# Optimization experiments

Hardware: AMD Instinct MI355X
Metric: run time of the kernel (lower is better)

The kernel has to match this reference:

```python
import jax, jax.numpy as jnp
import numpy as np

GROUPS = 32
HEADS = 8
EPS = 1e-5


def setup_inputs() -> dict:
    key = jax.random.key(0)
    ks = jax.random.split(key, 3)
    b, c, h, w = 8, 512, 32, 32
    x = jax.random.normal(ks[0], (b, c, h, w), dtype=jnp.float32)
    gn_w = jnp.ones((c,), jnp.float32)
    gn_b = jnp.zeros((c,), jnp.float32)
    qkv_w = jax.random.normal(ks[1], (3 * c, c), dtype=jnp.float32) * (1.0 / np.sqrt(c))
    qkv_b = jnp.zeros((3 * c,), jnp.float32)
    proj_w = jax.random.normal(ks[2], (c, c), dtype=jnp.float32) * (1.0 / np.sqrt(c))
    proj_b = jnp.zeros((c,), jnp.float32)
    return {"x": x, "gn_w": gn_w, "gn_b": gn_b, "qkv_w": qkv_w,
            "qkv_b": qkv_b, "proj_w": proj_w, "proj_b": proj_b}


def group_norm(x, weight, bias):
    b, c, h, w = x.shape
    xg = x.reshape(b, GROUPS, c // GROUPS, h, w)
    mean = xg.mean(axis=(2, 3, 4), keepdims=True)
    var = xg.var(axis=(2, 3, 4), keepdims=True)
    xn = ((xg - mean) * jax.lax.rsqrt(var + EPS)).reshape(b, c, h, w)
    return xn * weight[None, :, None, None] + bias[None, :, None, None]


def reference(x, gn_w, gn_b, qkv_w, qkv_b, proj_w, proj_b):
    b, c, h, w = x.shape
    dh = c // HEADS
    xn = group_norm(x, gn_w, gn_b)
    # 1x1 conv == per-pixel linear: (b,c,h,w) x (3c,c) -> (b,3c,h,w)
    qkv = jnp.einsum('bchw,oc->bohw', xn, qkv_w) + qkv_b[None, :, None, None]
    qkv = qkv.reshape(b, 3, HEADS, dh, h * w)  # 'three' outermost, then heads, head_dim
    q, k, v = qkv[:, 0], qkv[:, 1], qkv[:, 2]  # (b, heads, dh, hw)
    scale = dh ** (-0.5)
    attn = jax.nn.softmax(jnp.einsum('bhci,bhcj->bhij', q, k) * scale, axis=-1)
    out = jnp.einsum('bhij,bhcj->bhci', attn, v)  # (b, heads, dh, hw)
    out = out.reshape(b, c, h, w)
    out = jnp.einsum('bchw,oc->bohw', out, proj_w) + proj_b[None, :, None, None]
    return x + out
```

## Files before the change

### kernel.cpp

```cpp
#include <hip/hip_runtime.h>
#include <cstdint>
#include <cstddef>

#define BATCH 8
#define CCH   512
#define SSP   1024
#define NH    8
#define DH    64
#define O3    1536

typedef __bf16 bf16x8 __attribute__((ext_vector_type(8)));
typedef float  f32x4  __attribute__((ext_vector_type(4)));

__device__ __forceinline__ unsigned short f2bf(float f) {
    unsigned u = __builtin_bit_cast(unsigned, f);
    unsigned r = u + 0x7fffu + ((u >> 16) & 1u);
    return (unsigned short)(r >> 16);
}

__device__ __forceinline__ unsigned pk2bf(float lo, float hi) {
    unsigned ul = __builtin_bit_cast(unsigned, lo) + 0x8000u;
    unsigned uh = __builtin_bit_cast(unsigned, hi) + 0x8000u;
    return __builtin_amdgcn_perm(uh, ul, 0x07060302u);
}

__device__ __forceinline__ bf16x8 ld8(const unsigned short* p) {
    uint4 u = *(const uint4*)p;
    return __builtin_bit_cast(bf16x8, u);
}

__global__ __launch_bounds__(256) void wconv(const float* __restrict__ src,
                                             unsigned short* __restrict__ dst,
                                             int n4) {
    int i = blockIdx.x * 256 + threadIdx.x;
    if (i < n4) {
        float4 v = ((const float4*)src)[i];
        ushort4 o;
        o.x = f2bf(v.x); o.y = f2bf(v.y); o.z = f2bf(v.z); o.w = f2bf(v.w);
        ((ushort4*)dst)[i] = o;
    }
}

__global__ __launch_bounds__(256) void groupnorm_t(const float* __restrict__ x,
                                                   const float* __restrict__ gw,
                                                   const float* __restrict__ gb,
                                                   unsigned short* __restrict__ xnt) {
    int blk = blockIdx.x;
    int b = blk >> 5, g = blk & 31;
    const float4* xp = (const float4*)(x + (size_t)(b * CCH + g * 16) * SSP);
    int t = threadIdx.x;

    float4 vals[16];
    float sum = 0.f, ss = 0.f;
#pragma unroll
    for (int i = 0; i < 16; i++) {
        float4 v = xp[i * 256 + t];
        vals[i] = v;
        sum += (v.x + v.y) + (v.z + v.w);
        ss  += (v.x * v.x + v.y * v.y) + (v.z * v.z + v.w * v.w);
    }
#pragma unroll
    for (int o = 32; o; o >>= 1) {
        sum += __shfl_xor(sum, o, 64);
        ss  += __shfl_xor(ss,  o, 64);
    }
    __shared__ float red[8];
    if ((t & 63) == 0) { red[(t >> 6) * 2] = sum; red[(t >> 6) * 2 + 1] = ss; }
    __syncthreads();
    sum = red[0] + red[2] + red[4] + red[6];
    ss  = red[1] + red[3] + red[5] + red[7];

    float mean = sum * (1.f / 16384.f);
    float var  = ss * (1.f / 16384.f) - mean * mean;
    float rstd = rsqrtf(var + 1e-5f);

    __shared__ unsigned short tile[16][1032];
#pragma unroll
    for (int i = 0; i < 16; i++) {
        int f4 = i * 256 + t;
        int c = f4 >> 8;
        int s = (f4 & 255) * 4;
        float wsc = gw[g * 16 + c] * rstd;
        float bia = gb[g * 16 + c] - mean * wsc;
        float4 v = vals[i];
        tile[c][s + 0] = f2bf(v.x * wsc + bia);
        tile[c][s + 1] = f2bf(v.y * wsc + bia);
        tile[c][s + 2] = f2bf(v.z * wsc + bia);
        tile[c][s + 3] = f2bf(v.w * wsc + bia);
    }
    __syncthreads();

    int c2 = (t & 7) * 2, sr = t >> 3;
    unsigned short* outbase = xnt + (size_t)b * SSP * CCH + g * 16 + c2;
#pragma unroll
    for (int i = 0; i < 32; i++) {
        int s = i * 32 + sr;
        unsigned v = (unsigned)tile[c2][s] | ((unsigned)tile[c2 + 1][s] << 16);
        *(unsigned*)(outbase + (size_t)s * CCH) = v;
    }
}

__global__ __launch_bounds__(256) void gemm_qkv(const unsigned short* __restrict__ Aall,
                                                const unsigned short* __restrict__ Bw,
                                                const float* __restrict__ bias,
                                                unsigned short* __restrict__ Call) {
    const int K = 512;
    int bz = blockIdx.z;
    const unsigned short* A = Aall + (size_t)bz * SSP * CCH;
    unsigned short* Cp = Call + (size_t)bz * SSP * O3;
    int m0 = blockIdx.x * 128, n0 = blockIdx.y * 128;

    __shared__ unsigned short As[128][40], Bs[128][40];
    int t = threadIdx.x, wave = t >> 6, lane = t & 63;
    int quad = lane >> 4, l16 = lane & 15;
    int wm = (wave & 1) * 64, wn = (wave >> 1) * 64;

    f32x4 acc[4][4];
#pragma unroll
    for (int i = 0; i < 4; i++)
#pragma unroll
        for (int j = 0; j < 4; j++) acc[i][j] = f32x4{0.f, 0.f, 0.f, 0.f};

    int srow = t >> 2, scg = (t & 3) * 8;
    for (int k0 = 0; k0 < K; k0 += 32) {
        __syncthreads();
        *(uint4*)&As[srow][scg]      = *(const uint4*)(A  + (size_t)(m0 + srow) * K + k0 + scg);
        *(uint4*)&As[srow + 64][scg] = *(const uint4*)(A  + (size_t)(m0 + srow + 64) * K + k0 + scg);
        *(uint4*)&Bs[srow][scg]      = *(const uint4*)(Bw + (size_t)(n0 + srow) * K + k0 + scg);
        *(uint4*)&Bs[srow + 64][scg] = *(const uint4*)(Bw + (size_t)(n0 + srow + 64) * K + k0 + scg);
        __syncthreads();
        bf16x8 af[4], bfr[4];
#pragma unroll
        for (int i = 0; i < 4; i++) {
            af[i]  = ld8(&As[wm + i * 16 + l16][quad * 8]);
            bfr[i] = ld8(&Bs[wn + i * 16 + l16][quad * 8]);
        }
#pragma unroll
        for (int i = 0; i < 4; i++)
#pragma unroll
            for (int j = 0; j < 4; j++)
                acc[i][j] = __builtin_amdgcn_mfma_f32_16x16x32_bf16(af[i], bfr[j], acc[i][j], 0, 0, 0);
    }
#pragma unroll
    for (int i = 0; i < 4; i++)
#pragma unroll
        for (int j = 0; j < 4; j++) {
            int col = n0 + wn + j * 16 + l16;
            float bv = bias[col];
#pragma unroll
            for (int r = 0; r < 4; r++) {
                int row = m0 + wm + i * 16 + quad * 4 + r;
                Cp[(size_t)row * O3 + col] = f2bf(acc[i][j][r] + bv);
            }
        }
}

__global__ __launch_bounds__(256) void gemm_proj(const unsigned short* __restrict__ Pw,
                                                 const unsigned short* __restrict__ Oall,
                                                 const float* __restrict__ bias,
                                                 const float* __restrict__ xres,
                                                 float* __restrict__ Out) {
    const int K = 512;
    int bz = blockIdx.z;
    const unsigned short* Bv = Oall + (size_t)bz * SSP * CCH;
    int m0 = blockIdx.x * 128, n0 = blockIdx.y * 128;

    __shared__ unsigned short As[128][40], Bs[128][40];
    int t = threadIdx.x, wave = t >> 6, lane = t & 63;
    int quad = lane >> 4, l16 = lane & 15;
    int wm = (wave & 1) * 64, wn = (wave >> 1) * 64;

    f32x4 acc[4][4];
#pragma unroll
    for (int i = 0; i < 4; i++)
#pragma unroll
        for (int j = 0; j < 4; j++) acc[i][j] = f32x4{0.f, 0.f, 0.f, 0.f};

    int srow = t >> 2, scg = (t & 3) * 8;
    for (int k0 = 0; k0 < K; k0 += 32) {
        __syncthreads();
        *(uint4*)&As[srow][scg]      = *(const uint4*)(Pw + (size_t)(m0 + srow) * K + k0 + scg);
        *(uint4*)&As[srow + 64][scg] = *(const uint4*)(Pw + (size_t)(m0 + srow + 64) * K + k0 + scg);
        *(uint4*)&Bs[srow][scg]      = *(const uint4*)(Bv + (size_t)(n0 + srow) * K + k0 + scg);
        *(uint4*)&Bs[srow + 64][scg] = *(const uint4*)(Bv + (size_t)(n0 + srow + 64) * K + k0 + scg);
        __syncthreads();
        bf16x8 af[4], bfr[4];
#pragma unroll
        for (int i = 0; i < 4; i++) {
            af[i]  = ld8(&As[wm + i * 16 + l16][quad * 8]);
            bfr[i] = ld8(&Bs[wn + i * 16 + l16][quad * 8]);
        }
#pragma unroll
        for (int i = 0; i < 4; i++)
#pragma unroll
            for (int j = 0; j < 4; j++)
                acc[i][j] = __builtin_amdgcn_mfma_f32_16x16x32_bf16(af[i], bfr[j], acc[i][j], 0, 0, 0);
    }
#pragma unroll
    for (int i = 0; i < 4; i++)
#pragma unroll
        for (int j = 0; j < 4; j++) {
            int col = n0 + wn + j * 16 + l16;
#pragma unroll
            for (int r = 0; r < 4; r++) {
                int row = m0 + wm + i * 16 + quad * 4 + r;
                size_t idx = (size_t)bz * CCH * SSP + (size_t)row * SSP + col;
                Out[idx] = xres[idx] + acc[i][j][r] + bias[row];
            }
        }
}

__global__ __launch_bounds__(256) void vtrans(const unsigned short* __restrict__ qkvt,
                                              unsigned short* __restrict__ vt) {
    int j0 = blockIdx.x * 64;
    int bh = blockIdx.y;
    int b = bh >> 3, h = bh & 7;
    __shared__ unsigned short tl[64][72];
    int t = threadIdx.x;
#pragma unroll
    for (int p = 0; p < 2; p++) {
        int jr = p * 32 + (t >> 3), c8 = (t & 7) * 8;
        *(uint4*)&tl[jr][c8] =
            *(const uint4*)(qkvt + ((size_t)b * SSP + j0 + jr) * O3 + 2 * CCH + h * DH + c8);
    }
    __syncthreads();
#pragma unroll
    for (int p = 0; p < 2; p++) {
        int cr = p * 32 + (t >> 3), j8 = (t & 7) * 8;
        unsigned short vv[8];
#pragma unroll
        for (int i = 0; i < 8; i++) vv[i] = tl[j8 + i][cr];
        uint4 pack;
        pack.x = (unsigned)vv[0] | ((unsigned)vv[1] << 16);
        pack.y = (unsigned)vv[2] | ((unsigned)vv[3] << 16);
        pack.z = (unsigned)vv[4] | ((unsigned)vv[5] << 16);
        pack.w = (unsigned)vv[6] | ((unsigned)vv[7] << 16);
        *(uint4*)(vt + ((size_t)bh * DH + cr) * SSP + j0 + j8) = pack;
    }
}

__global__ __launch_bounds__(256, 4) void attn(const unsigned short* __restrict__ qkvt,
                                               const unsigned short* __restrict__ vt,
                                               unsigned short* __restrict__ ot) {
    int i0 = blockIdx.x * 64;
    int bh = blockIdx.y;
    int b = bh >> 3, h = bh & 7;

    __shared__ unsigned short Ks[128][72];
    __shared__ unsigned short Vs[64][136];

    int t = threadIdx.x, wave = t >> 6, lane = t & 63;
    int quad = lane >> 4, l16 = lane & 15;
    const float c1 = 0.125f * 1.44269504f;

    unsigned short* Ps = &Ks[0][0] + wave * (16 * 136);

    bf16x8 qf[2];
    {
        const unsigned short* qp =
            qkvt + ((size_t)b * SSP + i0 + wave * 16 + l16) * O3 + h * DH + quad * 8;
        qf[0] = ld8(qp);
        qf[1] = ld8(qp + 32);
    }

    f32x4 Oa[4];
#pragma unroll
    for (int i = 0; i < 4; i++) Oa[i] = f32x4{0.f, 0.f, 0.f, 0.f};
    float m_run = -INFINITY, l_run = 0.f;

    int jr = t >> 3, c8 = (t & 7) * 8;
    int cr = t >> 4, j8 = (t & 15) * 8;

    for (int jb = 0; jb < 8; jb++) {
        int j0 = jb * 128;
        __syncthreads();
#pragma unroll
        for (int p = 0; p < 4; p++) {
            int row = p * 32 + jr;
            *(uint4*)&Ks[row][c8] =
                *(const uint4*)(qkvt + ((size_t)b * SSP + j0 + row) * O3 + CCH + h * DH + c8);
        }
#pragma unroll
        for (int p = 0; p < 4; p++) {
            *(uint4*)&Vs[p * 16 + cr][j8] =
                *(const uint4*)(vt + ((size_t)bh * DH + p * 16 + cr) * SSP + j0 + j8);
        }
        __syncthreads();

        f32x4 sc[8];
#pragma unroll
        for (int tj = 0; tj < 8; tj++) sc[tj] = f32x4{0.f, 0.f, 0.f, 0.f};
#pragma unroll
        for (int kc = 0; kc < 2; kc++)
#pragma unroll
            for (int tj = 0; tj < 8; tj++) {
                bf16x8 kf = ld8(&Ks[tj * 16 + l16][kc * 32 + quad * 8]);
                sc[tj] = __builtin_amdgcn_mfma_f32_16x16x32_bf16(kf, qf[kc], sc[tj], 0, 0, 0);
            }

        float m = sc[0][0];
#pragma unroll
        for (int tj = 0; tj < 8; tj++)
#pragma unroll
            for (int r = 0; r < 4; r++) m = fmaxf(m, sc[tj][r]);
        m = fmaxf(m, __shfl_xor(m, 16, 64));
        m = fmaxf(m, __shfl_xor(m, 32, 64));
        float mn = fmaxf(m_run, m);
        float alpha = __builtin_amdgcn_exp2f(c1 * (m_run - mn));
        m_run = mn;
        float cm = c1 * mn;
        float rs = 0.f;
#pragma unroll
        for (int tj = 0; tj < 8; tj++)
#pragma unroll
            for (int r = 0; r < 4; r++) {
                float p = __builtin_amdgcn_exp2f(c1 * sc[tj][r] - cm);
                sc[tj][r] = p;
                rs += p;
            }
        rs += __shfl_xor(rs, 16, 64);
        rs += __shfl_xor(rs, 32, 64);
        l_run = l_run * alpha + rs;

        __syncthreads();

#pragma unroll
        for (int tj = 0; tj < 8; tj++) {
            uint2 d;
            d.x = pk2bf(sc[tj][0], sc[tj][1]);
            d.y = pk2bf(sc[tj][2], sc[tj][3]);
            *(uint2*)&Ps[l16 * 136 + tj * 16 + quad * 4] = d;
        }

#pragma unroll
        for (int tc = 0; tc < 4; tc++)
#pragma unroll
            for (int r = 0; r < 4; r++) Oa[tc][r] *= alpha;
#pragma unroll
        for (int kj = 0; kj < 4; kj++) {
            bf16x8 pf = ld8(&Ps[l16 * 136 + kj * 32 + quad * 8]);
#pragma unroll
            for (int tc = 0; tc < 4; tc++) {
                bf16x8 vf = ld8(&Vs[tc * 16 + l16][kj * 32 + quad * 8]);
                Oa[tc] = __builtin_amdgcn_mfma_f32_16x16x32_bf16(vf, pf, Oa[tc], 0, 0, 0);
            }
        }
    }

    float rl = 1.f / l_run;
    int i = i0 + wave * 16 + l16;
    unsigned short* ob = ot + ((size_t)b * SSP + i) * CCH + h * DH;
#pragma unroll
    for (int tc = 0; tc < 4; tc++) {
        uint2 d;
        d.x = pk2bf(Oa[tc][0] * rl, Oa[tc][1] * rl);
        d.y = pk2bf(Oa[tc][2] * rl, Oa[tc][3] * rl);
        *(uint2*)(ob + tc * 16 + quad * 4) = d;
    }
}

extern "C" void kernel_launch(void* const* d_in, const int* in_sizes, int n_in,
                              void* d_out, int out_size, void* d_ws, size_t ws_size,
                              hipStream_t stream) {
    const float* x      = (const float*)d_in[0];
    const float* gn_w   = (const float*)d_in[1];
    const float* gn_b   = (const float*)d_in[2];
    const float* qkv_w  = (const float*)d_in[3];
    const float* qkv_b  = (const float*)d_in[4];
    const float* proj_w = (const float*)d_in[5];
    const float* proj_b = (const float*)d_in[6];
    float* out = (float*)d_out;

    char* ws = (char*)d_ws;
    unsigned short* xnt   = (unsigned short*)(ws);
    unsigned short* qw_bf = (unsigned short*)(ws + 8388608);
    unsigned short* pw_bf = (unsigned short*)(ws + 9961472);
    unsigned short* qkvt  = (unsigned short*)(ws + 10485760);
    unsigned short* vt    = (unsigned short*)(ws + 35651584);
    unsigned short* otb   = (unsigned short*)(ws + 44040192);

    wconv<<<dim3(768), dim3(256), 0, stream>>>(qkv_w, qw_bf, 786432 / 4);
    wconv<<<dim3(256), dim3(256), 0, stream>>>(proj_w, pw_bf, 262144 / 4);
    groupnorm_t<<<dim3(256), dim3(256), 0, stream>>>(x, gn_w, gn_b, xnt);
    gemm_qkv<<<dim3(8, 12, 8), dim3(256), 0, stream>>>(xnt, qw_bf, qkv_b, qkvt);
    vtrans<<<dim3(16, 64), dim3(256), 0, stream>>>(qkvt, vt);
    attn<<<dim3(16, 64), dim3(256), 0, stream>>>(qkvt, vt, otb);
    gemm_proj<<<dim3(4, 8, 8), dim3(256), 0, stream>>>(pw_bf, otb, proj_b, x, out);
}
```

Measured before the change: 177.8 us.

## Fuse V transpose into QKV GEMM, use direct-to-LDS loads, prefetch attention tiles

```diff
diff --git a/kernel.cpp b/kernel.cpp
--- a/kernel.cpp
+++ b/kernel.cpp
@@ -29,16 +29,25 @@
     return __builtin_bit_cast(bf16x8, u);
 }
 
-__global__ __launch_bounds__(256) void wconv(const float* __restrict__ src,
-                                             unsigned short* __restrict__ dst,
-                                             int n4) {
+__device__ __forceinline__ void glls16(const void* g, void* l) {
+    __builtin_amdgcn_global_load_lds(
+        (const __attribute__((address_space(1))) unsigned*)g,
+        (__attribute__((address_space(3))) unsigned*)l, 16, 0, 0);
+}
+
+__global__ __launch_bounds__(256) void wconv2(const float* __restrict__ s1,
+                                              unsigned short* __restrict__ d1, int n1,
+                                              const float* __restrict__ s2,
+                                              unsigned short* __restrict__ d2) {
     int i = blockIdx.x * 256 + threadIdx.x;
-    if (i < n4) {
-        float4 v = ((const float4*)src)[i];
-        ushort4 o;
-        o.x = f2bf(v.x); o.y = f2bf(v.y); o.z = f2bf(v.z); o.w = f2bf(v.w);
-        ((ushort4*)dst)[i] = o;
-    }
+    const float4* sp;
+    ushort4* dp;
+    if (i < n1) { sp = (const float4*)s1 + i; dp = (ushort4*)d1 + i; }
+    else        { sp = (const float4*)s2 + (i - n1); dp = (ushort4*)d2 + (i - n1); }
+    float4 v = *sp;
+    ushort4 o;
+    o.x = f2bf(v.x); o.y = f2bf(v.y); o.z = f2bf(v.z); o.w = f2bf(v.w);
+    *dp = o;
 }
 
 __global__ __launch_bounds__(256) void groupnorm_t(const float* __restrict__ x,
@@ -103,56 +112,90 @@
 __global__ __launch_bounds__(256) void gemm_qkv(const unsigned short* __restrict__ Aall,
                                                 const unsigned short* __restrict__ Bw,
                                                 const float* __restrict__ bias,
-                                                unsigned short* __restrict__ Call) {
+                                                unsigned short* __restrict__ Call,
+                                                unsigned short* __restrict__ vtout) {
     const int K = 512;
     int bz = blockIdx.z;
     const unsigned short* A = Aall + (size_t)bz * SSP * CCH;
-    unsigned short* Cp = Call + (size_t)bz * SSP * O3;
     int m0 = blockIdx.x * 128, n0 = blockIdx.y * 128;
 
-    __shared__ unsigned short As[128][40], Bs[128][40];
+    __shared__ unsigned short As[128 * 64], Bs[128 * 64];
     int t = threadIdx.x, wave = t >> 6, lane = t & 63;
     int quad = lane >> 4, l16 = lane & 15;
     int wm = (wave & 1) * 64, wn = (wave >> 1) * 64;
 
+    int lrow = lane >> 3;
+    int lc   = ((lane & 7) - lrow) & 7;
+    const unsigned short* Ag = A  + (size_t)(m0 + wave * 32 + lrow) * K + lc * 8;
+    const unsigned short* Bg = Bw + (size_t)(n0 + wave * 32 + lrow) * K + lc * 8;
+    unsigned short* Asw = As + wave * 2048;
+    unsigned short* Bsw = Bs + wave * 2048;
+
     f32x4 acc[4][4];
 #pragma unroll
     for (int i = 0; i < 4; i++)
 #pragma unroll
         for (int j = 0; j < 4; j++) acc[i][j] = f32x4{0.f, 0.f, 0.f, 0.f};
 
-    int srow = t >> 2, scg = (t & 3) * 8;
-    for (int k0 = 0; k0 < K; k0 += 32) {
-        __syncthreads();
-        *(uint4*)&As[srow][scg]      = *(const uint4*)(A  + (size_t)(m0 + srow) * K + k0 + scg);
-        *(uint4*)&As[srow + 64][scg] = *(const uint4*)(A  + (size_t)(m0 + srow + 64) * K + k0 + scg);
-        *(uint4*)&Bs[srow][scg]      = *(const uint4*)(Bw + (size_t)(n0 + srow) * K + k0 + scg);
-        *(uint4*)&Bs[srow + 64][scg] = *(const uint4*)(Bw + (size_t)(n0 + srow + 64) * K + k0 + scg);
-        __syncthreads();
-        bf16x8 af[4], bfr[4];
+    int rowA = (wm + l16) * 64, rowB = (wn + l16) * 64;
+    int cph[2];
+#pragma unroll
+    for (int kc = 0; kc < 2; kc++) cph[kc] = ((quad + 4 * kc + l16) & 7) * 8;
+
+    for (int k0 = 0; k0 < K; k0 += 64) {
+        __syncthreads();
 #pragma unroll
         for (int i = 0; i < 4; i++) {
-            af[i]  = ld8(&As[wm + i * 16 + l16][quad * 8]);
-            bfr[i] = ld8(&Bs[wn + i * 16 + l16][quad * 8]);
-        }
+            glls16(Ag + (size_t)i * 8 * K + k0, Asw + i * 512);
+            glls16(Bg + (size_t)i * 8 * K + k0, Bsw + i * 512);
+        }
+        __syncthreads();
+#pragma unroll
+        for (int kc = 0; kc < 2; kc++) {
+            bf16x8 af[4], bfr[4];
+#pragma unroll
+            for (int i = 0; i < 4; i++) {
+                af[i]  = ld8(As + rowA + i * 1024 + cph[kc]);
+                bfr[i] = ld8(Bs + rowB + i * 1024 + cph[kc]);
+            }
+#pragma unroll
+            for (int i = 0; i < 4; i++)
+#pragma unroll
+                for (int j = 0; j < 4; j++)
+                    acc[i][j] = __builtin_amdgcn_mfma_f32_16x16x32_bf16(af[i], bfr[j], acc[i][j], 0, 0, 0);
+        }
+    }
+
+    if (n0 < 1024) {
+        unsigned short* Cp = Call + (size_t)bz * SSP * O3;
 #pragma unroll
         for (int i = 0; i < 4; i++)
 #pragma unroll
-            for (int j = 0; j < 4; j++)
-                acc[i][j] = __builtin_amdgcn_mfma_f32_16x16x32_bf16(af[i], bfr[j], acc[i][j], 0, 0, 0);
-    }
-#pragma unroll
-    for (int i = 0; i < 4; i++)
+            for (int j = 0; j < 4; j++) {
+                int col = n0 + wn + j * 16 + l16;
+                float bv = bias[col];
+#pragma unroll
+                for (int r = 0; r < 4; r++) {
+                    int row = m0 + wm + i * 16 + quad * 4 + r;
+                    Cp[(size_t)row * O3 + col] = f2bf(acc[i][j][r] + bv);
+                }
+            }
+    } else {
 #pragma unroll
         for (int j = 0; j < 4; j++) {
             int col = n0 + wn + j * 16 + l16;
             float bv = bias[col];
-#pragma unroll
-            for (int r = 0; r < 4; r++) {
-                int row = m0 + wm + i * 16 + quad * 4 + r;
-                Cp[(size_t)row * O3 + col] = f2bf(acc[i][j][r] + bv);
-            }
-        }
+            unsigned short* vp = vtout + ((size_t)bz * 512 + (col - 1024)) * SSP;
+#pragma unroll
+            for (int i = 0; i < 4; i++) {
+                int s = m0 + wm + i * 16 + quad * 4;
+                uint2 d;
+                d.x = pk2bf(acc[i][j][0] + bv, acc[i][j][1] + bv);
+                d.y = pk2bf(acc[i][j][2] + bv, acc[i][j][3] + bv);
+                *(uint2*)(vp + s) = d;
+            }
+        }
+    }
 }
 
 __global__ __launch_bounds__(256) void gemm_proj(const unsigned short* __restrict__ Pw,
@@ -165,36 +208,51 @@
     const unsigned short* Bv = Oall + (size_t)bz * SSP * CCH;
     int m0 = blockIdx.x * 128, n0 = blockIdx.y * 128;
 
-    __shared__ unsigned short As[128][40], Bs[128][40];
+    __shared__ unsigned short As[128 * 64], Bs[128 * 64];
     int t = threadIdx.x, wave = t >> 6, lane = t & 63;
     int quad = lane >> 4, l16 = lane & 15;
     int wm = (wave & 1) * 64, wn = (wave >> 1) * 64;
 
+    int lrow = lane >> 3;
+    int lc   = ((lane & 7) - lrow) & 7;
+    const unsigned short* Ag = Pw + (size_t)(m0 + wave * 32 + lrow) * K + lc * 8;
+    const unsigned short* Bg = Bv + (size_t)(n0 + wave * 32 + lrow) * K + lc * 8;
+    unsigned short* Asw = As + wave * 2048;
+    unsigned short* Bsw = Bs + wave * 2048;
+
     f32x4 acc[4][4];
 #pragma unroll
     for (int i = 0; i < 4; i++)
 #pragma unroll
         for (int j = 0; j < 4; j++) acc[i][j] = f32x4{0.f, 0.f, 0.f, 0.f};
 
-    int srow = t >> 2, scg = (t & 3) * 8;
-    for (int k0 = 0; k0 < K; k0 += 32) {
-        __syncthreads();
-        *(uint4*)&As[srow][scg]      = *(const uint4*)(Pw + (size_t)(m0 + srow) * K + k0 + scg);
-        *(uint4*)&As[srow + 64][scg] = *(const uint4*)(Pw + (size_t)(m0 + srow + 64) * K + k0 + scg);
-        *(uint4*)&Bs[srow][scg]      = *(const uint4*)(Bv + (size_t)(n0 + srow) * K + k0 + scg);
-        *(uint4*)&Bs[srow + 64][scg] = *(const uint4*)(Bv + (size_t)(n0 + srow + 64) * K + k0 + scg);
-        __syncthreads();
-        bf16x8 af[4], bfr[4];
+    int rowA = (wm + l16) * 64, rowB = (wn + l16) * 64;
+    int cph[2];
+#pragma unroll
+    for (int kc = 0; kc < 2; kc++) cph[kc] = ((quad + 4 * kc + l16) & 7) * 8;
+
+    for (int k0 = 0; k0 < K; k0 += 64) {
+        __syncthreads();
 #pragma unroll
         for (int i = 0; i < 4; i++) {
-            af[i]  = ld8(&As[wm + i * 16 + l16][quad * 8]);
-            bfr[i] = ld8(&Bs[wn + i * 16 + l16][quad * 8]);
-        }
-#pragma unroll
-        for (int i = 0; i < 4; i++)
-#pragma unroll
-            for (int j = 0; j < 4; j++)
-                acc[i][j] = __builtin_amdgcn_mfma_f32_16x16x32_bf16(af[i], bfr[j], acc[i][j], 0, 0, 0);
+            glls16(Ag + (size_t)i * 8 * K + k0, Asw + i * 512);
+            glls16(Bg + (size_t)i * 8 * K + k0, Bsw + i * 512);
+        }
+        __syncthreads();
+#pragma unroll
+        for (int kc = 0; kc < 2; kc++) {
+            bf16x8 af[4], bfr[4];
+#pragma unroll
+            for (int i = 0; i < 4; i++) {
+                af[i]  = ld8(As + rowA + i * 1024 + cph[kc]);
+                bfr[i] = ld8(Bs + rowB + i * 1024 + cph[kc]);
+            }
+#pragma unroll
+            for (int i = 0; i < 4; i++)
+#pragma unroll
+                for (int j = 0; j < 4; j++)
+                    acc[i][j] = __builtin_amdgcn_mfma_f32_16x16x32_bf16(af[i], bfr[j], acc[i][j], 0, 0, 0);
+        }
     }
 #pragma unroll
     for (int i = 0; i < 4; i++)
@@ -208,35 +266,6 @@
                 Out[idx] = xres[idx] + acc[i][j][r] + bias[row];
             }
         }
-}
-
-__global__ __launch_bounds__(256) void vtrans(const unsigned short* __restrict__ qkvt,
-                                              unsigned short* __restrict__ vt) {
-    int j0 = blockIdx.x * 64;
-    int bh = blockIdx.y;
-    int b = bh >> 3, h = bh & 7;
-    __shared__ unsigned short tl[64][72];
-    int t = threadIdx.x;
-#pragma unroll
-    for (int p = 0; p < 2; p++) {
-        int jr = p * 32 + (t >> 3), c8 = (t & 7) * 8;
-        *(uint4*)&tl[jr][c8] =
-            *(const uint4*)(qkvt + ((size_t)b * SSP + j0 + jr) * O3 + 2 * CCH + h * DH + c8);
-    }
-    __syncthreads();
-#pragma unroll
-    for (int p = 0; p < 2; p++) {
-        int cr = p * 32 + (t >> 3), j8 = (t & 7) * 8;
-        unsigned short vv[8];
-#pragma unroll
-        for (int i = 0; i < 8; i++) vv[i] = tl[j8 + i][cr];
-        uint4 pack;
-        pack.x = (unsigned)vv[0] | ((unsigned)vv[1] << 16);
-        pack.y = (unsigned)vv[2] | ((unsigned)vv[3] << 16);
-        pack.z = (unsigned)vv[4] | ((unsigned)vv[5] << 16);
-        pack.w = (unsigned)vv[6] | ((unsigned)vv[7] << 16);
-        *(uint4*)(vt + ((size_t)bh * DH + cr) * SSP + j0 + j8) = pack;
-    }
 }
 
 __global__ __launch_bounds__(256, 4) void attn(const unsigned short* __restrict__ qkvt,
@@ -270,22 +299,31 @@
 
     int jr = t >> 3, c8 = (t & 7) * 8;
     int cr = t >> 4, j8 = (t & 15) * 8;
+    const unsigned short* kg = qkvt + ((size_t)b * SSP + jr) * O3 + CCH + h * DH + c8;
+    const unsigned short* vg = vt + ((size_t)bh * DH + cr) * SSP + j8;
+
+    uint4 kreg[4], vreg[4];
+#pragma unroll
+    for (int p = 0; p < 4; p++) kreg[p] = *(const uint4*)(kg + (size_t)p * 32 * O3);
+#pragma unroll
+    for (int p = 0; p < 4; p++) vreg[p] = *(const uint4*)(vg + (size_t)p * 16 * SSP);
 
     for (int jb = 0; jb < 8; jb++) {
-        int j0 = jb * 128;
-        __syncthreads();
-#pragma unroll
-        for (int p = 0; p < 4; p++) {
-            int row = p * 32 + jr;
-            *(uint4*)&Ks[row][c8] =
-                *(const uint4*)(qkvt + ((size_t)b * SSP + j0 + row) * O3 + CCH + h * DH + c8);
-        }
-#pragma unroll
-        for (int p = 0; p < 4; p++) {
-            *(uint4*)&Vs[p * 16 + cr][j8] =
-                *(const uint4*)(vt + ((size_t)bh * DH + p * 16 + cr) * SSP + j0 + j8);
-        }
-        __syncthreads();
+        __syncthreads();
+#pragma unroll
+        for (int p = 0; p < 4; p++) *(uint4*)&Ks[p * 32 + jr][c8] = kreg[p];
+#pragma unroll
+        for (int p = 0; p < 4; p++) *(uint4*)&Vs[p * 16 + cr][j8] = vreg[p];
+        __syncthreads();
+
+        if (jb < 7) {
+            const unsigned short* kg2 = kg + (size_t)(jb + 1) * 128 * O3;
+            const unsigned short* vg2 = vg + (size_t)(jb + 1) * 128;
+#pragma unroll
+            for (int p = 0; p < 4; p++) kreg[p] = *(const uint4*)(kg2 + (size_t)p * 32 * O3);
+#pragma unroll
+            for (int p = 0; p < 4; p++) vreg[p] = *(const uint4*)(vg2 + (size_t)p * 16 * SSP);
+        }
 
         f32x4 sc[8];
 #pragma unroll
@@ -379,11 +417,9 @@
     unsigned short* vt    = (unsigned short*)(ws + 35651584);
     unsigned short* otb   = (unsigned short*)(ws + 44040192);
 
-    wconv<<<dim3(768), dim3(256), 0, stream>>>(qkv_w, qw_bf, 786432 / 4);
-    wconv<<<dim3(256), dim3(256), 0, stream>>>(proj_w, pw_bf, 262144 / 4);
+    wconv2<<<dim3(1024), dim3(256), 0, stream>>>(qkv_w, qw_bf, 196608, proj_w, pw_bf);
     groupnorm_t<<<dim3(256), dim3(256), 0, stream>>>(x, gn_w, gn_b, xnt);
-    gemm_qkv<<<dim3(8, 12, 8), dim3(256), 0, stream>>>(xnt, qw_bf, qkv_b, qkvt);
-    vtrans<<<dim3(16, 64), dim3(256), 0, stream>>>(qkvt, vt);
+    gemm_qkv<<<dim3(8, 12, 8), dim3(256), 0, stream>>>(xnt, qw_bf, qkv_b, qkvt, vt);
     attn<<<dim3(16, 64), dim3(256), 0, stream>>>(qkvt, vt, otb);
     gemm_proj<<<dim3(4, 8, 8), dim3(256), 0, stream>>>(pw_bf, otb, proj_b, x, out);
 }
```

After: 232.0 us. 30.5% more time.
